# Kernel tuning notes

Hardware: AMD Instinct MI355X
Metric: run time of the kernel (lower is better)

The kernel has to match this reference:

```python
import jax, jax.numpy as jnp
import numpy as np

B, DIM, HH, WW = 8, 512, 64, 64
HEADS, DH = 8, 64
INNER = HEADS * DH
EPS = 1e-5  # ChanLayerNorm2D eps


def _chan_norm(x, g, b):
    # channel-wise layernorm over axis 1 (biased variance, like torch.var(unbiased=False))
    m = jnp.mean(x, axis=1, keepdims=True)
    v = jnp.mean((x - m) ** 2, axis=1, keepdims=True)
    return (x - m) / jnp.sqrt(v + EPS) * g + b


def _l2norm(x):
    # F.normalize(dim=1), eps=1e-12
    n = jnp.sqrt(jnp.sum(x * x, axis=1, keepdims=True))
    return x / jnp.maximum(n, 1e-12)


def setup_inputs() -> dict:
    key = jax.random.key(0)
    ks = jax.random.split(key, 10)
    sc = 1.0 / np.sqrt(DIM)
    return {
        "context": jax.random.normal(ks[0], (B, DIM, HH, WW), jnp.float32),
        "query_source": jax.random.normal(ks[1], (B, DIM, HH, WW), jnp.float32),
        "ctx_g": jnp.ones((1, DIM, 1, 1), jnp.float32),
        "ctx_b": jnp.zeros((1, DIM, 1, 1), jnp.float32),
        "qs_g": jnp.ones((1, DIM, 1, 1), jnp.float32),
        "qs_b": jnp.zeros((1, DIM, 1, 1), jnp.float32),
        "w_q": jax.random.normal(ks[2], (INNER, DIM), jnp.float32) * sc,
        "w_kv": jax.random.normal(ks[3], (2 * INNER, DIM), jnp.float32) * sc,
        "w_out": jax.random.normal(ks[4], (DIM, INNER), jnp.float32) * (1.0 / np.sqrt(INNER)),
        "gamma": jax.random.normal(ks[5], (1,), jnp.float32) * 0.5,
    }


def reference(context, query_source, ctx_g, ctx_b, qs_g, qs_b, w_q, w_kv, w_out, gamma):
    b, c, height, width = query_source.shape
    kh = int(height ** 0.5)  # default height_top_k
    kw = int(width ** 0.5)   # default width_top_k

    ctx = _chan_norm(context, ctx_g, ctx_b)
    qs = _chan_norm(query_source, qs_g, qs_b)

    # 1x1 convs as GEMMs
    kv = jnp.einsum('oi,bihw->bohw', w_kv, ctx)
    k, v = jnp.split(kv, 2, axis=1)
    q = jnp.einsum('oi,bihw->bohw', w_q, qs)

    def fold(t):  # b (h c) H W -> (b h) c H W
        return t.reshape(b, HEADS, DH, height, width).reshape(b * HEADS, DH, height, width)

    q, k, v = fold(q), fold(k), fold(v)
    q, k = _l2norm(q), _l2norm(k)

    # dual pruning (kh < height and kw < width here)
    q_abs = jnp.abs(q)
    k_abs = jnp.abs(k)
    q_probe = jnp.sum(q_abs, axis=(2, 3))            # (bh, c)

    # height selection
    k_height = jnp.sum(k_abs, axis=3)                # (bh, c, H)
    score_r = jnp.einsum('bc,bch->bh', q_probe, k_height)
    _, idx_h = jax.lax.top_k(score_r, kh)            # (bh, kh)
    k = jnp.take_along_axis(k, idx_h[:, None, :, None], axis=2)
    v = jnp.take_along_axis(v, idx_h[:, None, :, None], axis=2)

    # width selection (scores use pre-height-gather k_abs, as in original)
    k_width = jnp.sum(k_abs, axis=2)                 # (bh, c, W)
    score_c = jnp.einsum('bc,bcw->bw', q_probe, k_width)
    _, idx_w = jax.lax.top_k(score_c, kw)            # (bh, kw)
    k = jnp.take_along_axis(k, idx_w[:, None, None, :], axis=3)
    v = jnp.take_along_axis(v, idx_w[:, None, None, :], axis=3)

    def flat(t):  # (bh) d h w -> (bh) (h w) d
        bh, d, h_, w_ = t.shape
        return t.transpose(0, 2, 3, 1).reshape(bh, h_ * w_, d)

    qf, kf, vf = flat(q), flat(k), flat(v)
    attn = jax.nn.softmax(jnp.einsum('bid,bjd->bij', qf, kf), axis=-1)
    out = jnp.einsum('bij,bjd->bid', attn, vf)       # (bh, H*W, d)

    out = out.reshape(b, HEADS, height, width, DH).transpose(0, 1, 4, 2, 3)
    out = out.reshape(b, INNER, height, width)
    out = jnp.einsum('oi,bihw->bohw', w_out, out)
    return gamma[0] * out + qs
```

## Files before the change

### kernel.cpp

```cpp
#include <hip/hip_runtime.h>
#include <math.h>

#define HW 4096
#define DIM 512

typedef __attribute__((ext_vector_type(8))) short short8;
typedef __attribute__((ext_vector_type(4))) float f32x4;

__device__ inline unsigned short f2bf(float f) {
    unsigned int u = __float_as_uint(f);
    u += 0x7fff + ((u >> 16) & 1);
    return (unsigned short)(u >> 16);
}
__device__ inline float bf2f(unsigned short h) {
    return __uint_as_float(((unsigned int)h) << 16);
}
__device__ inline unsigned pack2(float a, float b) {
    return (unsigned)f2bf(a) | ((unsigned)f2bf(b) << 16);
}

__global__ void prep_weights(const float* __restrict__ w_q, const float* __restrict__ w_kv,
                             const float* __restrict__ w_out,
                             const float* __restrict__ ctx_g, const float* __restrict__ ctx_b,
                             const float* __restrict__ qs_g, const float* __restrict__ qs_b,
                             unsigned short* __restrict__ wq_b, unsigned short* __restrict__ wk_b,
                             unsigned short* __restrict__ wo_b, float* __restrict__ wv_g,
                             float* __restrict__ Avec, float* __restrict__ Cvec)
{
    int blk = blockIdx.x;
    int widx = blk >> 9;
    int o = blk & 511;
    int tid = threadIdx.x;
    const float *src, *g = nullptr, *beta = nullptr;
    if (widx == 0)      { src = w_q  + (size_t)o * DIM; g = qs_g;  beta = qs_b; }
    else if (widx == 1) { src = w_kv + (size_t)o * DIM; g = ctx_g; beta = ctx_b; }
    else if (widx == 2) { src = w_kv + (size_t)(512 + o) * DIM; g = ctx_g; beta = ctx_b; }
    else                { src = w_out + (size_t)o * DIM; }
    float a = 0.f, c = 0.f;
    for (int i = tid; i < DIM; i += 256) {
        float w = src[i];
        if (widx == 3) { wo_b[(size_t)o * DIM + i] = f2bf(w); continue; }
        float wg = w * g[i];
        if (widx == 0)      wq_b[(size_t)o * DIM + i] = f2bf(wg);
        else if (widx == 1) wk_b[(size_t)o * DIM + i] = f2bf(wg);
        else                wv_g[(size_t)o * DIM + i] = wg;
        a += wg; c += w * beta[i];
    }
    if (widx == 3) return;
    __shared__ float sa[256], sc[256];
    sa[tid] = a; sc[tid] = c;
    __syncthreads();
    for (int s = 128; s > 0; s >>= 1) {
        if (tid < s) { sa[tid] += sa[tid + s]; sc[tid] += sc[tid + s]; }
        __syncthreads();
    }
    if (tid == 0) { Avec[widx * 512 + o] = sa[0]; Cvec[widx * 512 + o] = sc[0]; }
}

__global__ __launch_bounds__(256) void conv_stats(
    const float* __restrict__ ctx, const float* __restrict__ qs,
    unsigned short* __restrict__ ctx_t, unsigned short* __restrict__ qs_t,
    float* __restrict__ ctx_m, float* __restrict__ ctx_r,
    float* __restrict__ qs_m, float* __restrict__ qs_r)
{
    int which = blockIdx.z;
    int b = blockIdx.y;
    int p0 = blockIdx.x * 64;
    const float* X = (which ? qs : ctx) + (size_t)b * DIM * HW;
    unsigned short* Xt = (which ? qs_t : ctx_t) + (size_t)b * HW * DIM;
    int tid = threadIdx.x;
    int p = p0 + (tid & 63);
    int q4 = tid >> 6;
    const float* col = X + p;
    unsigned short* orow = Xt + (size_t)p * DIM;
    float s = 0.f, ss = 0.f;
    for (int i0 = q4 * 128; i0 < q4 * 128 + 128; i0 += 8) {
        float v[8];
#pragma unroll
        for (int j = 0; j < 8; j++) {
            v[j] = col[(size_t)(i0 + j) * HW];
            s += v[j]; ss = fmaf(v[j], v[j], ss);
        }
        uint4 pk;
        pk.x = pack2(v[0], v[1]);
        pk.y = pack2(v[2], v[3]);
        pk.z = pack2(v[4], v[5]);
        pk.w = pack2(v[6], v[7]);
        *(uint4*)(orow + i0) = pk;
    }
    __shared__ float sbuf[256], ssbuf[256];
    sbuf[tid] = s; ssbuf[tid] = ss;
    __syncthreads();
    if (tid < 64) {
        float st  = sbuf[tid] + sbuf[tid + 64] + sbuf[tid + 128] + sbuf[tid + 192];
        float sst = ssbuf[tid] + ssbuf[tid + 64] + ssbuf[tid + 128] + ssbuf[tid + 192];
        float m = st * (1.0f / DIM);
        float var = sst * (1.0f / DIM) - m * m;
        float r = 1.0f / sqrtf(var + 1e-5f);
        int pix = b * HW + p0 + tid;
        if (which == 0) { ctx_m[pix] = m; ctx_r[pix] = r; }
        else            { qs_m[pix]  = m; qs_r[pix]  = r; }
    }
}

template<int MODE>
__global__ __launch_bounds__(256) void gemm_mfma(
    const unsigned short* __restrict__ Wb, const unsigned short* __restrict__ Xt,
    float* __restrict__ Y, unsigned short* __restrict__ Ybf,
    const float* __restrict__ mean, const float* __restrict__ rstd,
    const float* __restrict__ Arow, const float* __restrict__ Crow,
    float* __restrict__ probe,
    const float* __restrict__ qsrc, const float* __restrict__ g,
    const float* __restrict__ beta, const float* __restrict__ gammaPtr)
{
    int b = blockIdx.z;
    int n0 = blockIdx.x * 128;
    int m0 = blockIdx.y * 128;
    const unsigned short* Xb = Xt + (size_t)b * HW * DIM;
    __shared__ uint4 AsBuf[512];
    __shared__ uint4 BsBuf[512];
    unsigned short* As = (unsigned short*)AsBuf;
    unsigned short* Bs = (unsigned short*)BsBuf;
    int tid = threadIdx.x;
    int lane = tid & 63;
    int wave = tid >> 6;
    int wm = (wave >> 1) * 64;
    int wn = (wave & 1) * 64;
    int quad = lane >> 4;
    int l16 = lane & 15;

    int r0 = tid >> 2, c0 = (tid & 3) * 8;
    const uint4* gA0 = (const uint4*)(Wb + (size_t)(m0 + r0) * DIM + c0);
    const uint4* gA1 = (const uint4*)(Wb + (size_t)(m0 + 64 + r0) * DIM + c0);
    const uint4* gB0 = (const uint4*)(Xb + (size_t)(n0 + r0) * DIM + c0);
    const uint4* gB1 = (const uint4*)(Xb + (size_t)(n0 + 64 + r0) * DIM + c0);

    f32x4 acc[4][4];
#pragma unroll
    for (int i = 0; i < 4; i++)
#pragma unroll
        for (int j = 0; j < 4; j++) acc[i][j] = (f32x4){0.f, 0.f, 0.f, 0.f};

    uint4 ra0 = gA0[0], ra1 = gA1[0], rb0 = gB0[0], rb1 = gB1[0];
    for (int kt = 0; kt < 16; kt++) {
        ((uint4*)As)[tid] = ra0;
        ((uint4*)As)[tid + 256] = ra1;
        ((uint4*)Bs)[tid] = rb0;
        ((uint4*)Bs)[tid + 256] = rb1;
        __syncthreads();
        if (kt < 15) {
            ra0 = gA0[(kt + 1) * 4]; ra1 = gA1[(kt + 1) * 4];
            rb0 = gB0[(kt + 1) * 4]; rb1 = gB1[(kt + 1) * 4];
        }
        short8 af[4], bfr[4];
#pragma unroll
        for (int i = 0; i < 4; i++)
            af[i] = *(const short8*)(As + (wm + i * 16 + l16) * 32 + quad * 8);
#pragma unroll
        for (int j = 0; j < 4; j++)
            bfr[j] = *(const short8*)(Bs + (wn + j * 16 + l16) * 32 + quad * 8);
#pragma unroll
        for (int i = 0; i < 4; i++)
#pragma unroll
            for (int j = 0; j < 4; j++)
                acc[i][j] = __builtin_amdgcn_mfma_f32_16x16x32_bf16(af[i], bfr[j], acc[i][j], 0, 0, 0);
        __syncthreads();
    }

    if (MODE < 2) {
        float pa[4][4] = {};
#pragma unroll
        for (int j = 0; j < 4; j++) {
            int n = n0 + wn + j * 16 + l16;
            int pix = b * HW + n;
            float mn = mean[pix], rs = rstd[pix];
            float y[4][4];
            float s2 = 0.f;
#pragma unroll
            for (int i = 0; i < 4; i++) {
                int mb = m0 + wm + i * 16 + quad * 4;
#pragma unroll
                for (int r = 0; r < 4; r++) {
                    float v = rs * (acc[i][j][r] - mn * Arow[mb + r]) + Crow[mb + r];
                    y[i][r] = v;
                    s2 = fmaf(v, v, s2);
                }
            }
            s2 += __shfl_xor(s2, 16, 64);
            s2 += __shfl_xor(s2, 32, 64);
            float inv = 1.0f / fmaxf(sqrtf(s2), 1e-12f);
            unsigned short* orow = Ybf + (size_t)(b * HW + n) * 512 + m0 + wm + quad * 4;
#pragma unroll
            for (int i = 0; i < 4; i++) {
                float v0 = y[i][0] * inv, v1 = y[i][1] * inv;
                float v2 = y[i][2] * inv, v3 = y[i][3] * inv;
                uint2 pk; pk.x = pack2(v0, v1); pk.y = pack2(v2, v3);
                *(uint2*)(orow + i * 16) = pk;
                pa[i][0] += fabsf(v0); pa[i][1] += fabsf(v1);
                pa[i][2] += fabsf(v2); pa[i][3] += fabsf(v3);
            }
        }
#pragma unroll
        for (int i = 0; i < 4; i++)
#pragma unroll
            for (int r = 0; r < 4; r++) {
                float v = pa[i][r];
                v += __shfl_xor(v, 1, 64);
                v += __shfl_xor(v, 2, 64);
                v += __shfl_xor(v, 4, 64);
                v += __shfl_xor(v, 8, 64);
                pa[i][r] = v;
            }
        if (l16 == 0) {
#pragma unroll
            for (int i = 0; i < 4; i++)
#pragma unroll
                for (int r = 0; r < 4; r++) {
                    int m = m0 + wm + i * 16 + quad * 4 + r;
                    if (MODE == 0) atomicAdd(&probe[b * 512 + m], pa[i][r]);
                    else atomicAdd(&probe[(size_t)(b * 512 + m) * 64 + ((n0 + wn) >> 6)], pa[i][r]);
                }
        }
    } else {
        float* Yb = Y + (size_t)b * DIM * HW;
        float gamma = gammaPtr[0];
        const float* qb = qsrc + (size_t)b * DIM * HW;
#pragma unroll
        for (int j = 0; j < 4; j++) {
            int n = n0 + wn + j * 16 + l16;
            int pix = b * HW + n;
            float mn = mean[pix], rs = rstd[pix];
#pragma unroll
            for (int i = 0; i < 4; i++) {
                int mb = m0 + wm + i * 16 + quad * 4;
#pragma unroll
                for (int r = 0; r < 4; r++) {
                    int m = mb + r;
                    float qn = (qb[(size_t)m * HW + n] - mn) * rs * g[m] + beta[m];
                    Yb[(size_t)m * HW + n] = gamma * acc[i][j][r] + qn;
                }
            }
        }
    }
}

__global__ void kws_kernel(const unsigned short* __restrict__ kbf, float* __restrict__ kws)
{
    int blk = blockIdx.x;
    int b = blk >> 6, w = blk & 63;
    int t = threadIdx.x;
    float a0 = 0.f, a1 = 0.f;
    for (int h = 0; h < 64; h++) {
        const unsigned short* row = kbf + (size_t)(b * HW + h * 64 + w) * 512;
        a0 += fabsf(bf2f(row[t]));
        a1 += fabsf(bf2f(row[t + 256]));
    }
    kws[(size_t)(b * 512 + t) * 64 + w] = a0;
    kws[(size_t)(b * 512 + t + 256) * 64 + w] = a1;
}

__global__ void score_topk(const float* __restrict__ qp, const float* __restrict__ khs,
                           const float* __restrict__ kws, int* __restrict__ idx_h, int* __restrict__ idx_w)
{
    int bh = blockIdx.x;
    int lane = threadIdx.x;
    float sr = 0.f, sc = 0.f;
    for (int c = 0; c < 64; c++) {
        float q = qp[bh * 64 + c];
        sr = fmaf(q, khs[(size_t)(bh * 64 + c) * 64 + lane], sr);
        sc = fmaf(q, kws[(size_t)(bh * 64 + c) * 64 + lane], sc);
    }
    float v = sr;
    for (int it = 0; it < 8; it++) {
        float bv = v; int bi = lane;
        for (int off = 1; off < 64; off <<= 1) {
            float ov = __shfl_xor(bv, off, 64);
            int oi = __shfl_xor(bi, off, 64);
            if (ov > bv || (ov == bv && oi < bi)) { bv = ov; bi = oi; }
        }
        if (lane == 0) idx_h[bh * 8 + it] = bi;
        if (lane == bi) v = -INFINITY;
    }
    v = sc;
    for (int it = 0; it < 8; it++) {
        float bv = v; int bi = lane;
        for (int off = 1; off < 64; off <<= 1) {
            float ov = __shfl_xor(bv, off, 64);
            int oi = __shfl_xor(bi, off, 64);
            if (ov > bv || (ov == bv && oi < bi)) { bv = ov; bi = oi; }
        }
        if (lane == 0) idx_w[bh * 8 + it] = bi;
        if (lane == bi) v = -INFINITY;
    }
}

__global__ void gather_kv(const unsigned short* __restrict__ kbf, const unsigned short* __restrict__ ctx_t,
                          const float* __restrict__ wv_g, const float* __restrict__ Av, const float* __restrict__ Cv,
                          const float* __restrict__ ctx_m, const float* __restrict__ ctx_r,
                          const int* __restrict__ idx_h, const int* __restrict__ idx_w,
                          unsigned short* __restrict__ kg, unsigned short* __restrict__ vgt)
{
    int blk = blockIdx.x;
    int bh = blk >> 6, j = blk & 63;
    int h = idx_h[bh * 8 + (j >> 3)];
    int w = idx_w[bh * 8 + (j & 7)];
    int p = h * 64 + w;
    int b = bh >> 3, head = bh & 7;
    int d = threadIdx.x;
    kg[(size_t)blk * 64 + d] = kbf[(size_t)(b * HW + p) * 512 + head * 64 + d];
    __shared__ float cx[DIM];
    const unsigned short* crow = ctx_t + (size_t)(b * HW + p) * 512;
    short8 cv = ((const short8*)crow)[d];
#pragma unroll
    for (int u = 0; u < 8; u++) cx[d * 8 + u] = bf2f((unsigned short)cv[u]);
    __syncthreads();
    int o = head * 64 + d;
    const float* wrow = wv_g + (size_t)o * DIM;
    float acc = 0.f;
    for (int i = 0; i < DIM; i++) acc = fmaf(wrow[i], cx[i], acc);
    int pix = b * HW + p;
    float v = ctx_r[pix] * (acc - ctx_m[pix] * Av[o]) + Cv[o];
    vgt[((size_t)bh * 64 + d) * 64 + j] = f2bf(v);
}

#define PROW 72
__global__ __launch_bounds__(256) void attn_mfma(
    const unsigned short* __restrict__ qbf, const unsigned short* __restrict__ kg,
    const unsigned short* __restrict__ vgt, unsigned short* __restrict__ abuf)
{
    int bh = blockIdx.y;
    int b = bh >> 3, head = bh & 7;
    int tid = threadIdx.x;
    int lane = tid & 63, wave = tid >> 6;
    int g = lane >> 4, l16 = lane & 15;
    int p0 = blockIdx.x * 256 + wave * 64;

    __shared__ unsigned short Plds[4][64 * PROW];
    unsigned short* P = Plds[wave];

    const unsigned short* kgb = kg + (size_t)bh * 4096;
    const unsigned short* vtb = vgt + (size_t)bh * 4096;
    const unsigned short* qb = qbf + (size_t)(b * HW) * 512 + head * 64;

    short8 Qf[4][2];
#pragma unroll
    for (int j = 0; j < 4; j++)
#pragma unroll
        for (int t = 0; t < 2; t++)
            Qf[j][t] = *(const short8*)(qb + (size_t)(p0 + j * 16 + l16) * 512 + t * 32 + g * 8);

    f32x4 S[4][4];
#pragma unroll
    for (int i = 0; i < 4; i++)
#pragma unroll
        for (int j = 0; j < 4; j++) S[i][j] = (f32x4){0.f, 0.f, 0.f, 0.f};
#pragma unroll
    for (int t = 0; t < 2; t++) {
        short8 Kf[4];
#pragma unroll
        for (int i = 0; i < 4; i++)
            Kf[i] = *(const short8*)(kgb + (i * 16 + l16) * 64 + t * 32 + g * 8);
#pragma unroll
        for (int i = 0; i < 4; i++)
#pragma unroll
            for (int j = 0; j < 4; j++)
                S[i][j] = __builtin_amdgcn_mfma_f32_16x16x32_bf16(Kf[i], Qf[j][t], S[i][j], 0, 0, 0);
    }

    float inv[4];
#pragma unroll
    for (int j = 0; j < 4; j++) {
        float e[4][4];
        float s = 0.f;
#pragma unroll
        for (int i = 0; i < 4; i++)
#pragma unroll
            for (int r = 0; r < 4; r++) { e[i][r] = __expf(S[i][j][r]); s += e[i][r]; }
        s += __shfl_xor(s, 16, 64);
        s += __shfl_xor(s, 32, 64);
        inv[j] = 1.0f / s;
        int row = j * 16 + l16;
#pragma unroll
        for (int i = 0; i < 4; i++) {
            uint2 pk;
            pk.x = pack2(e[i][0], e[i][1]);
            pk.y = pack2(e[i][2], e[i][3]);
            *(uint2*)(P + row * PROW + i * 16 + g * 4) = pk;
        }
    }

    f32x4 O[4][4];
#pragma unroll
    for (int i = 0; i < 4; i++)
#pragma unroll
        for (int j = 0; j < 4; j++) O[i][j] = (f32x4){0.f, 0.f, 0.f, 0.f};
#pragma unroll
    for (int t = 0; t < 2; t++) {
        short8 Vf[4], Pf[4];
#pragma unroll
        for (int i = 0; i < 4; i++)
            Vf[i] = *(const short8*)(vtb + (i * 16 + l16) * 64 + t * 32 + g * 8);
#pragma unroll
        for (int j = 0; j < 4; j++)
            Pf[j] = *(const short8*)(P + (j * 16 + l16) * PROW + t * 32 + g * 8);
#pragma unroll
        for (int i = 0; i < 4; i++)
#pragma unroll
            for (int j = 0; j < 4; j++)
                O[i][j] = __builtin_amdgcn_mfma_f32_16x16x32_bf16(Vf[i], Pf[j], O[i][j], 0, 0, 0);
    }

    unsigned short* ob = abuf + (size_t)(b * HW) * 512 + head * 64;
#pragma unroll
    for (int j = 0; j < 4; j++) {
        int p = p0 + j * 16 + l16;
#pragma unroll
        for (int i = 0; i < 4; i++) {
            uint2 pk;
            pk.x = pack2(O[i][j][0] * inv[j], O[i][j][1] * inv[j]);
            pk.y = pack2(O[i][j][2] * inv[j], O[i][j][3] * inv[j]);
            *(uint2*)(ob + (size_t)p * 512 + i * 16 + g * 4) = pk;
        }
    }
}

extern "C" void kernel_launch(void* const* d_in, const int* in_sizes, int n_in,
                              void* d_out, int out_size, void* d_ws, size_t ws_size,
                              hipStream_t stream)
{
    (void)in_sizes; (void)n_in; (void)out_size; (void)ws_size;
    const float* ctx   = (const float*)d_in[0];
    const float* qs    = (const float*)d_in[1];
    const float* ctx_g = (const float*)d_in[2];
    const float* ctx_b = (const float*)d_in[3];
    const float* qs_g  = (const float*)d_in[4];
    const float* qs_b  = (const float*)d_in[5];
    const float* w_q   = (const float*)d_in[6];
    const float* w_kv  = (const float*)d_in[7];
    const float* w_out = (const float*)d_in[8];
    const float* gamma = (const float*)d_in[9];
    float* out = (float*)d_out;

    char* base = (char*)d_ws;
    unsigned short* ctx_t = (unsigned short*)base;
    unsigned short* abuf  = ctx_t;
    unsigned short* qs_t  = (unsigned short*)(base + ((size_t)32 << 20));
    unsigned short* kbf   = qs_t;
    unsigned short* qbf   = (unsigned short*)(base + ((size_t)64 << 20));
    char* tail = base + ((size_t)96 << 20);
    unsigned short* wq_b = (unsigned short*)tail;
    unsigned short* wk_b = wq_b + 262144;
    unsigned short* wo_b = wk_b + 262144;
    float* wv_g  = (float*)(wo_b + 262144);
    float* Avec  = wv_g + 262144;
    float* Cvec  = Avec + 1536;
    float* ctx_m = Cvec + 1536;
    float* ctx_r = ctx_m + 32768;
    float* qs_m  = ctx_r + 32768;
    float* qs_r  = qs_m + 32768;
    float* qp    = qs_r + 32768;
    float* khs   = qp + 4096;
    float* kws   = khs + 262144;
    int*   idxh  = (int*)(kws + 262144);
    int*   idxw  = idxh + 512;
    unsigned short* kg  = (unsigned short*)(idxw + 512);
    unsigned short* vgt = kg + 262144;

    hipMemsetAsync(qp, 0, 4096 * sizeof(float), stream);
    hipMemsetAsync(khs, 0, 262144 * sizeof(float), stream);

    prep_weights<<<2048, 256, 0, stream>>>(w_q, w_kv, w_out, ctx_g, ctx_b, qs_g, qs_b,
                                           wq_b, wk_b, wo_b, wv_g, Avec, Cvec);
    conv_stats<<<dim3(64, 8, 2), 256, 0, stream>>>(ctx, qs, ctx_t, qs_t,
                                                   ctx_m, ctx_r, qs_m, qs_r);
    gemm_mfma<0><<<dim3(32, 4, 8), 256, 0, stream>>>(wq_b, qs_t, nullptr, qbf, qs_m, qs_r,
                                                     Avec, Cvec, qp, nullptr, nullptr, nullptr, nullptr);
    gemm_mfma<1><<<dim3(32, 4, 8), 256, 0, stream>>>(wk_b, ctx_t, nullptr, kbf, ctx_m, ctx_r,
                                                     Avec + 512, Cvec + 512, khs, nullptr, nullptr, nullptr, nullptr);
    kws_kernel<<<512, 256, 0, stream>>>(kbf, kws);
    score_topk<<<64, 64, 0, stream>>>(qp, khs, kws, idxh, idxw);
    gather_kv<<<4096, 64, 0, stream>>>(kbf, ctx_t, wv_g, Avec + 1024, Cvec + 1024,
                                       ctx_m, ctx_r, idxh, idxw, kg, vgt);
    attn_mfma<<<dim3(16, 64), 256, 0, stream>>>(qbf, kg, vgt, abuf);
    gemm_mfma<2><<<dim3(32, 4, 8), 256, 0, stream>>>(wo_b, abuf, out, nullptr, qs_m, qs_r,
                                                     nullptr, nullptr, nullptr, qs, qs_g, qs_b, gamma);
}
```

Measured before the change: 481.2 us.

## Stage transposes through LDS, use direct global-to-LDS loads, vectorize kws reduction

The channel-stats transpose kernel now writes bf16 output through a swizzled LDS tile, so global stores are contiguous rows instead of strided per-pixel writes. The MFMA GEMM loads its A/B tiles with global_load_lds directly into shared memory, removing register staging. This also drops the previous register prefetch overlap. The width-sum kernel reads 16-byte vectors across four height groups and reduces in LDS, replacing scalar 2-byte loads.

```diff
diff --git a/kernel.cpp b/kernel.cpp
--- a/kernel.cpp
+++ b/kernel.cpp
@@ -17,6 +17,12 @@
 }
 __device__ inline unsigned pack2(float a, float b) {
     return (unsigned)f2bf(a) | ((unsigned)f2bf(b) << 16);
+}
+
+__device__ inline void gld16(const void* g, void* lds) {
+    __builtin_amdgcn_global_load_lds(
+        (const __attribute__((address_space(1))) unsigned int*)g,
+        (__attribute__((address_space(3))) unsigned int*)lds, 16, 0, 0);
 }
 
 __global__ void prep_weights(const float* __restrict__ w_q, const float* __restrict__ w_kv,
@@ -69,26 +75,43 @@
     const float* X = (which ? qs : ctx) + (size_t)b * DIM * HW;
     unsigned short* Xt = (which ? qs_t : ctx_t) + (size_t)b * HW * DIM;
     int tid = threadIdx.x;
-    int p = p0 + (tid & 63);
+    int p = tid & 63;
     int q4 = tid >> 6;
-    const float* col = X + p;
-    unsigned short* orow = Xt + (size_t)p * DIM;
+    const float* col = X + p0 + p;
+
+    __shared__ uint4 tile[64 * 32];
+    __shared__ float sbuf[256], ssbuf[256];
+
     float s = 0.f, ss = 0.f;
-    for (int i0 = q4 * 128; i0 < q4 * 128 + 128; i0 += 8) {
-        float v[8];
-#pragma unroll
-        for (int j = 0; j < 8; j++) {
-            v[j] = col[(size_t)(i0 + j) * HW];
-            s += v[j]; ss = fmaf(v[j], v[j], ss);
-        }
-        uint4 pk;
-        pk.x = pack2(v[0], v[1]);
-        pk.y = pack2(v[2], v[3]);
-        pk.z = pack2(v[4], v[5]);
-        pk.w = pack2(v[6], v[7]);
-        *(uint4*)(orow + i0) = pk;
-    }
-    __shared__ float sbuf[256], ssbuf[256];
+    for (int chunk = 0; chunk < 2; chunk++) {
+        for (int si = 0; si < 8; si++) {
+            int cgl = q4 * 8 + si;
+            int c = chunk * 256 + cgl * 8;
+            float v[8];
+#pragma unroll
+            for (int j = 0; j < 8; j++) {
+                v[j] = col[(size_t)(c + j) * HW];
+                s += v[j]; ss = fmaf(v[j], v[j], ss);
+            }
+            uint4 pk;
+            pk.x = pack2(v[0], v[1]);
+            pk.y = pack2(v[2], v[3]);
+            pk.z = pack2(v[4], v[5]);
+            pk.w = pack2(v[6], v[7]);
+            tile[p * 32 + (cgl ^ (p & 15))] = pk;
+        }
+        __syncthreads();
+        int pr = tid >> 2, c2 = tid & 3;
+        unsigned short* orow = Xt + (size_t)(p0 + pr) * 512 + chunk * 256;
+#pragma unroll
+        for (int si = 0; si < 8; si++) {
+            int cgl = c2 + si * 4;
+            uint4 d = tile[pr * 32 + (cgl ^ (pr & 15))];
+            *(uint4*)(orow + cgl * 8) = d;
+        }
+        __syncthreads();
+    }
+
     sbuf[tid] = s; ssbuf[tid] = ss;
     __syncthreads();
     if (tid < 64) {
@@ -124,16 +147,17 @@
     int tid = threadIdx.x;
     int lane = tid & 63;
     int wave = tid >> 6;
+    int wbase = tid & 192;
     int wm = (wave >> 1) * 64;
     int wn = (wave & 1) * 64;
     int quad = lane >> 4;
     int l16 = lane & 15;
 
     int r0 = tid >> 2, c0 = (tid & 3) * 8;
-    const uint4* gA0 = (const uint4*)(Wb + (size_t)(m0 + r0) * DIM + c0);
-    const uint4* gA1 = (const uint4*)(Wb + (size_t)(m0 + 64 + r0) * DIM + c0);
-    const uint4* gB0 = (const uint4*)(Xb + (size_t)(n0 + r0) * DIM + c0);
-    const uint4* gB1 = (const uint4*)(Xb + (size_t)(n0 + 64 + r0) * DIM + c0);
+    const unsigned short* pA0 = Wb + (size_t)(m0 + r0) * DIM + c0;
+    const unsigned short* pA1 = Wb + (size_t)(m0 + 64 + r0) * DIM + c0;
+    const unsigned short* pB0 = Xb + (size_t)(n0 + r0) * DIM + c0;
+    const unsigned short* pB1 = Xb + (size_t)(n0 + 64 + r0) * DIM + c0;
 
     f32x4 acc[4][4];
 #pragma unroll
@@ -141,17 +165,13 @@
 #pragma unroll
         for (int j = 0; j < 4; j++) acc[i][j] = (f32x4){0.f, 0.f, 0.f, 0.f};
 
-    uint4 ra0 = gA0[0], ra1 = gA1[0], rb0 = gB0[0], rb1 = gB1[0];
     for (int kt = 0; kt < 16; kt++) {
-        ((uint4*)As)[tid] = ra0;
-        ((uint4*)As)[tid + 256] = ra1;
-        ((uint4*)Bs)[tid] = rb0;
-        ((uint4*)Bs)[tid + 256] = rb1;
+        gld16(pA0, AsBuf + wbase);
+        gld16(pA1, AsBuf + 256 + wbase);
+        gld16(pB0, BsBuf + wbase);
+        gld16(pB1, BsBuf + 256 + wbase);
+        pA0 += 32; pA1 += 32; pB0 += 32; pB1 += 32;
         __syncthreads();
-        if (kt < 15) {
-            ra0 = gA0[(kt + 1) * 4]; ra1 = gA1[(kt + 1) * 4];
-            rb0 = gB0[(kt + 1) * 4]; rb1 = gB1[(kt + 1) * 4];
-        }
         short8 af[4], bfr[4];
 #pragma unroll
         for (int i = 0; i < 4; i++)
@@ -244,19 +264,34 @@
     }
 }
 
-__global__ void kws_kernel(const unsigned short* __restrict__ kbf, float* __restrict__ kws)
+__global__ __launch_bounds__(256) void kws_kernel(const unsigned short* __restrict__ kbf,
+                                                  float* __restrict__ kws)
 {
     int blk = blockIdx.x;
     int b = blk >> 6, w = blk & 63;
-    int t = threadIdx.x;
-    float a0 = 0.f, a1 = 0.f;
-    for (int h = 0; h < 64; h++) {
-        const unsigned short* row = kbf + (size_t)(b * HW + h * 64 + w) * 512;
-        a0 += fabsf(bf2f(row[t]));
-        a1 += fabsf(bf2f(row[t + 256]));
-    }
-    kws[(size_t)(b * 512 + t) * 64 + w] = a0;
-    kws[(size_t)(b * 512 + t + 256) * 64 + w] = a1;
+    int tid = threadIdx.x;
+    int c8 = tid & 63;
+    int hq = tid >> 6;
+    float a[8] = {};
+    for (int hh = 0; hh < 16; hh++) {
+        const unsigned short* row = kbf + ((size_t)(b * HW + (hq * 16 + hh) * 64 + w)) * 512 + c8 * 8;
+        uint4 pk = *(const uint4*)row;
+        const unsigned short* u = (const unsigned short*)&pk;
+#pragma unroll
+        for (int j = 0; j < 8; j++) a[j] += fabsf(bf2f(u[j]));
+    }
+    __shared__ float red[512 * 4];
+#pragma unroll
+    for (int j = 0; j < 8; j++) red[(c8 * 8 + j) * 4 + hq] = a[j];
+    __syncthreads();
+    if (tid < 256) {
+        int c = tid;
+        float v0 = red[c * 4] + red[c * 4 + 1] + red[c * 4 + 2] + red[c * 4 + 3];
+        int c2 = tid + 256;
+        float v1 = red[c2 * 4] + red[c2 * 4 + 1] + red[c2 * 4 + 2] + red[c2 * 4 + 3];
+        kws[(size_t)(b * 512 + c) * 64 + w] = v0;
+        kws[(size_t)(b * 512 + c2) * 64 + w] = v1;
+    }
 }
 
 __global__ void score_topk(const float* __restrict__ qp, const float* __restrict__ khs,
```

New measurement: 449.6 us. 6.6% less time.
